# Kernel optimization log

Measured on AMD Instinct MI355X. Metric: run time of the kernel, lower is better.

The kernel has to match this reference:

```python
import jax, jax.numpy as jnp
import numpy as np
from jax import lax

H = 512   # hidden_size
R = 4     # read heads
W = 32    # memory word size
N = 64    # memory cells
B = 64    # batch
T = 256   # seq len
IFACE = R * W + 3 * W + 5 * R + 3      # 247
HID_C = H + IFACE                       # 759 controller LSTM hidden
IN_C = H + R * W                        # 640 controller LSTM input
EPS = 1e-6


def setup_inputs() -> dict:
    key = jax.random.key(0)
    ks = jax.random.split(key, 7)
    s = 0.05
    return {
        "x": jax.random.normal(ks[0], (B, T, H), jnp.float32),
        "Wih_e": jax.random.normal(ks[1], (4 * H, H), jnp.float32) * s,
        "Whh_e": jax.random.normal(ks[2], (4 * H, H), jnp.float32) * s,
        "b_e": jnp.zeros((4 * H,), jnp.float32),
        "Wih_c": jax.random.normal(ks[3], (4 * HID_C, IN_C), jnp.float32) * s,
        "Whh_c": jax.random.normal(ks[4], (4 * HID_C, HID_C), jnp.float32) * s,
        "b_c": jnp.zeros((4 * HID_C,), jnp.float32),
    }


def lstm_cell(xt, h, c, Wih, Whh, b):
    g = xt @ Wih.T + h @ Whh.T + b
    i, f, gg, o = jnp.split(g, 4, axis=-1)  # PyTorch gate order i,f,g,o
    c = jax.nn.sigmoid(f) * c + jax.nn.sigmoid(i) * jnp.tanh(gg)
    h = jax.nn.sigmoid(o) * jnp.tanh(c)
    return h, c


def content_weights(M, keys, strengths):
    # M: [B,N,W], keys: [B,K,W], strengths: [B,K] -> softmaxed similarity [B,K,N]
    Mn = M * lax.rsqrt(jnp.sum(M * M, -1, keepdims=True) + EPS)
    kn = keys * lax.rsqrt(jnp.sum(keys * keys, -1, keepdims=True) + EPS)
    sim = jnp.einsum('bkw,bnw->bkn', kn, Mn)
    return jax.nn.softmax(sim * strengths[..., None], axis=-1)


def reference(x, Wih_e, Whh_e, b_e, Wih_c, Whh_c, b_c):
    # ---- encoder LSTM over time ----
    def enc_step(carry, xt):
        h, c = carry
        h, c = lstm_cell(xt, h, c, Wih_e, Whh_e, b_e)
        return (h, c), h

    z = jnp.zeros((B, H), x.dtype)
    _, enc = lax.scan(enc_step, (z, z), x.transpose(1, 0, 2))  # [T,B,H]

    # ---- controller LSTM + DNC memory per timestep ----
    eye = jnp.eye(N, dtype=x.dtype)

    def dnc_step(carry, e_t):
        h, c, M, u, p, L, wr, ww, rv = carry
        x_t = jnp.concatenate([e_t, rv], axis=-1)          # [B, H + R*W]
        h, c = lstm_cell(x_t, h, c, Wih_c, Whh_c, b_c)
        out = h[:, :H]
        xi = h[:, H:]                                       # [B, IFACE]
        o = 0
        read_keys = jnp.tanh(xi[:, :R * W].reshape(B, R, W)); o = R * W
        read_str = jax.nn.softplus(xi[:, o:o + R]); o += R
        write_key = jnp.tanh(xi[:, o:o + W]).reshape(B, 1, W); o += W
        write_str = jax.nn.softplus(xi[:, o:o + 1]); o += 1
        erase = jax.nn.sigmoid(xi[:, o:o + W]); o += W
        write_vec = jnp.tanh(xi[:, o:o + W]); o += W
        free_g = jax.nn.sigmoid(xi[:, o:o + R]); o += R
        alloc_g = jax.nn.sigmoid(xi[:, o:o + 1]); o += 1
        write_g = jax.nn.sigmoid(xi[:, o:o + 1]); o += 1
        read_modes = jax.nn.softmax(xi[:, o:o + 3 * R].reshape(B, R, 3), -1)
        # usage + retention
        psi = jnp.prod(1.0 - free_g[..., None] * wr, axis=1)   # [B,N]
        u = (u + ww - u * ww) * psi
        # allocation weighting via sorted usage
        idx = jnp.argsort(u, axis=-1)
        su = jnp.take_along_axis(u, idx, -1)
        cp = jnp.concatenate([jnp.ones((B, 1), u.dtype), jnp.cumprod(su, -1)[:, :-1]], -1)
        a = jnp.take_along_axis((1.0 - su) * cp, jnp.argsort(idx, -1), -1)
        # write weighting
        cw = content_weights(M, write_key, write_str)[:, 0]    # [B,N]
        ww = write_g * (alloc_g * a + (1.0 - alloc_g) * cw)
        # memory write
        M = M * (1.0 - ww[..., None] * erase[:, None, :]) + ww[..., None] * write_vec[:, None, :]
        # temporal link + precedence
        L = (1.0 - ww[:, :, None] - ww[:, None, :]) * L + ww[:, :, None] * p[:, None, :]
        L = L * (1.0 - eye)
        p = (1.0 - jnp.sum(ww, -1, keepdims=True)) * p + ww
        # read weighting: backward, content, forward modes
        cr = content_weights(M, read_keys, read_str)           # [B,R,N]
        fw = jnp.einsum('bnm,brm->brn', L, wr)
        bw = jnp.einsum('bmn,brm->brn', L, wr)
        wr = read_modes[..., 0:1] * bw + read_modes[..., 1:2] * cr + read_modes[..., 2:3] * fw
        rv = jnp.einsum('brn,bnw->brw', wr, M).reshape(B, R * W)
        return (h, c, M, u, p, L, wr, ww, rv), out

    init = (
        jnp.zeros((B, HID_C), x.dtype), jnp.zeros((B, HID_C), x.dtype),
        jnp.zeros((B, N, W), x.dtype), jnp.zeros((B, N), x.dtype),
        jnp.zeros((B, N), x.dtype), jnp.zeros((B, N, N), x.dtype),
        jnp.zeros((B, R, N), x.dtype), jnp.zeros((B, N), x.dtype),
        jnp.zeros((B, R * W), x.dtype),
    )
    _, outs = lax.scan(dnc_step, init, enc)   # [T,B,H]
    return outs.transpose(1, 0, 2)            # dnc_encoded [B,T,H]
```

## Files before the change

kernel.cpp:

```cpp
#include <hip/hip_runtime.h>
#include <math.h>


#define EPSF 1e-6f

__device__ __forceinline__ float sigmoidf_(float x) { return 1.f / (1.f + expf(-x)); }
__device__ __forceinline__ float softplusf_(float x) {
    return (x > 0.f) ? x + log1pf(expf(-x)) : log1pf(expf(x));
}
__device__ __forceinline__ void stg_coh(float* p, float v) {
    __hip_atomic_store(p, v, __ATOMIC_RELAXED, __HIP_MEMORY_SCOPE_AGENT);
}
__device__ __forceinline__ void st_flag(int* p, int v) {
    __hip_atomic_store(p, v, __ATOMIC_RELAXED, __HIP_MEMORY_SCOPE_AGENT);
}
__device__ __forceinline__ int ld_flag(const int* p) {
    return __hip_atomic_load(p, __ATOMIC_RELAXED, __HIP_MEMORY_SCOPE_AGENT);
}
__device__ __forceinline__ void poll256(const int* f, int lane, int tgt) {
    const int* p = f + lane * 32;
    for (;;) {
        int a = ld_flag(p);
        int b = ld_flag(p + 64 * 32);
        int c = ld_flag(p + 128 * 32);
        int d = ld_flag(p + 192 * 32);
        if (__all(min(min(a, b), min(c, d)) >= tgt)) break;
        __builtin_amdgcn_s_sleep(2);
    }
}
__device__ __forceinline__ void pollg(const int* f, int lane, int tgt) {
    const int* p = f + (64 + lane) * 32;
    for (;;) {
        int a = ld_flag(p);
        int b = ld_flag(p + 64 * 32);
        int c = ld_flag(p + 128 * 32);
        if (__all(min(min(a, b), c) >= tgt)) break;
        __builtin_amdgcn_s_sleep(2);
    }
}
__device__ __forceinline__ void pollx(const int* f, int lane, int tgt) {
    const int* p = f + (192 + (lane < 62 ? lane : 61)) * 32;
    while (!__all(ld_flag(p) >= tgt)) __builtin_amdgcn_s_sleep(2);
}
__device__ __forceinline__ void pollm(const int* f2, int lane, int tgt) {
    while (!__all(ld_flag(f2 + lane * 32) >= tgt)) __builtin_amdgcn_s_sleep(2);
}

__global__ __launch_bounds__(256) void prep_weights(const float* __restrict__ Whh_c,
                                                    const float* __restrict__ Wih_c,
                                                    float* __restrict__ Wcat) {
    int idx = blockIdx.x * 256 + threadIdx.x;
    if (idx < 3036 * 896) {
        int r = idx / 896, j = idx - r * 896;
        float v;
        if (j < 759) v = Whh_c[r * 759 + j];
        else if (j < 768) v = 0.f;
        else v = Wih_c[r * 640 + 512 + (j - 768)];
        Wcat[idx] = v;
    }
}

__global__ __launch_bounds__(256, 2) void proj_gemm(const float* __restrict__ A,
                                                    const float* __restrict__ W,
                                                    const float* __restrict__ bias,
                                                    float* __restrict__ OUT, int Ncols,
                                                    int wstride, int arow_base, int arow_stride_t,
                                                    int arow_stride_b, int arowlen, int Mrows) {
    __shared__ float As[16 * 68];
    __shared__ float Ws[16 * 68];
    const int tid = threadIdx.x;
    const int ntile = blockIdx.x, mtile = blockIdx.y;
    const int tx = tid & 15, ty = tid >> 4;
    const int lr = tid >> 2;
    const int lk = (tid & 3) * 4;
    const size_t arow =
        (size_t)arow_base + (size_t)mtile * arow_stride_t + (size_t)lr * arow_stride_b;
    const float* aptr = A + arow * arowlen + lk;
    const int wn = ntile * 64 + lr;
    const bool wok = (wn < Ncols);
    const float* wptr = W + (size_t)(wok ? wn : 0) * wstride + lk;
    float acc[4][4] = {};
    for (int kt = 0; kt < 512; kt += 16) {
        float4 av = *(const float4*)(aptr + kt);
        float4 w4l = *(const float4*)(wptr + kt);
        if (!wok) w4l = make_float4(0.f, 0.f, 0.f, 0.f);
        __syncthreads();
        As[(lk + 0) * 68 + lr] = av.x;
        As[(lk + 1) * 68 + lr] = av.y;
        As[(lk + 2) * 68 + lr] = av.z;
        As[(lk + 3) * 68 + lr] = av.w;
        Ws[(lk + 0) * 68 + lr] = w4l.x;
        Ws[(lk + 1) * 68 + lr] = w4l.y;
        Ws[(lk + 2) * 68 + lr] = w4l.z;
        Ws[(lk + 3) * 68 + lr] = w4l.w;
        __syncthreads();
#pragma unroll
        for (int k = 0; k < 16; ++k) {
            float4 a4 = *(const float4*)&As[k * 68 + ty * 4];
            float4 w4 = *(const float4*)&Ws[k * 68 + tx * 4];
            acc[0][0] = fmaf(a4.x, w4.x, acc[0][0]);
            acc[0][1] = fmaf(a4.x, w4.y, acc[0][1]);
            acc[0][2] = fmaf(a4.x, w4.z, acc[0][2]);
            acc[0][3] = fmaf(a4.x, w4.w, acc[0][3]);
            acc[1][0] = fmaf(a4.y, w4.x, acc[1][0]);
            acc[1][1] = fmaf(a4.y, w4.y, acc[1][1]);
            acc[1][2] = fmaf(a4.y, w4.z, acc[1][2]);
            acc[1][3] = fmaf(a4.y, w4.w, acc[1][3]);
            acc[2][0] = fmaf(a4.z, w4.x, acc[2][0]);
            acc[2][1] = fmaf(a4.z, w4.y, acc[2][1]);
            acc[2][2] = fmaf(a4.z, w4.z, acc[2][2]);
            acc[2][3] = fmaf(a4.z, w4.w, acc[2][3]);
            acc[3][0] = fmaf(a4.w, w4.x, acc[3][0]);
            acc[3][1] = fmaf(a4.w, w4.y, acc[3][1]);
            acc[3][2] = fmaf(a4.w, w4.z, acc[3][2]);
            acc[3][3] = fmaf(a4.w, w4.w, acc[3][3]);
        }
    }
    const int col0 = ntile * 64 + tx * 4;
    const int row0 = mtile * 64 + ty * 4;
#pragma unroll
    for (int j = 0; j < 4; ++j) {
        int col = col0 + j;
        if (col < Ncols) {
            float bv = bias[col];
            float4 st = make_float4(acc[0][j] + bv, acc[1][j] + bv, acc[2][j] + bv,
                                    acc[3][j] + bv);
            *(float4*)&OUT[(size_t)col * Mrows + row0] = st;
        }
    }
}

__global__ __launch_bounds__(256) void enc_emit(const float* __restrict__ HSE,
                                                float* __restrict__ ENC, int t0) {
    const int tl = blockIdx.x, bgrp = blockIdx.y;
    const int c4 = threadIdx.x & 127, b = bgrp * 2 + (threadIdx.x >> 7);
    float4 v = *(const float4*)&HSE[(size_t)tl * 32768 + c4 * 256 + b * 4];
    *(float4*)&ENC[((size_t)(t0 + tl) * 64 + b) * 512 + c4 * 4] = v;
}
__global__ __launch_bounds__(256) void out_emit(const float* __restrict__ HS,
                                                float* __restrict__ OUT, int t0) {
    const int tl = blockIdx.x, bgrp = blockIdx.y;
    const int c4 = threadIdx.x & 127, b = bgrp * 2 + (threadIdx.x >> 7);
    float4 v = *(const float4*)&HS[(size_t)tl * 57344 + c4 * 256 + b * 4];
    *(float4*)&OUT[(size_t)b * 131072 + (size_t)(t0 + tl) * 512 + c4 * 4] = v;
}

__global__ __launch_bounds__(512, 1) void enc_seq(const float* __restrict__ Whh,
                                                  const float* __restrict__ XPT,
                                                  float* __restrict__ HSE,
                                                  float* __restrict__ CE, int M, int TC,
                                                  int* flags) {
    __shared__ float part[8 * 4 * 64];
    __shared__ float hstage[128 * 256];
    const int tid = threadIdx.x;
    const int bk = blockIdx.x;
    const int lane = tid & 63;
    const int wv = __builtin_amdgcn_readfirstlane(tid >> 6);
    const int q = wv & 3, cidx = wv >> 2;
    const int cell = bk + 256 * cidx;
    const float* __restrict__ w0 = Whh + ((size_t)(0 * 512 + cell)) * 512 + q * 128;
    const float* __restrict__ w1 = Whh + ((size_t)(1 * 512 + cell)) * 512 + q * 128;
    const float* __restrict__ w2 = Whh + ((size_t)(2 * 512 + cell)) * 512 + q * 128;
    const float* __restrict__ w3 = Whh + ((size_t)(3 * 512 + cell)) * 512 + q * 128;
    float c_reg = 0.f;
    if (q == 0) c_reg = CE[cell * 64 + lane];
    for (int tl = 0; tl < TC; ++tl) {
        const float* rslot = HSE + (size_t)((tl + TC - 1) % TC) * 32768;
        float* wslot = HSE + (size_t)tl * 32768;
        float x0 = 0.f, x1 = 0.f, x2 = 0.f, x3 = 0.f;
        if (q == 0) {
            const int m = tl * 64 + lane;
            x0 = XPT[(size_t)(0 * 512 + cell) * M + m];
            x1 = XPT[(size_t)(1 * 512 + cell) * M + m];
            x2 = XPT[(size_t)(2 * 512 + cell) * M + m];
            x3 = XPT[(size_t)(3 * 512 + cell) * M + m];
        }
        {
            float4* __restrict__ hs4 = (float4*)hstage;
            const float4* __restrict__ src4 = (const float4*)rslot;
#pragma unroll
            for (int k = 0; k < 16; ++k) hs4[tid + k * 512] = src4[tid + k * 512];
        }
        __syncthreads();
        float a0 = 0.f, a1 = 0.f, a2 = 0.f, a3 = 0.f;
        {
            const float4* __restrict__ hx = (const float4*)hstage + q * 32 * 64;
#pragma unroll 8
            for (int i = 0; i < 32; ++i) {
                float4 hv = hx[i * 64 + lane];
                float4 q0 = *(const float4*)&w0[i * 4];
                float4 q1 = *(const float4*)&w1[i * 4];
                float4 q2 = *(const float4*)&w2[i * 4];
                float4 q3 = *(const float4*)&w3[i * 4];
                a0 = fmaf(hv.x, q0.x, a0); a0 = fmaf(hv.y, q0.y, a0);
                a0 = fmaf(hv.z, q0.z, a0); a0 = fmaf(hv.w, q0.w, a0);
                a1 = fmaf(hv.x, q1.x, a1); a1 = fmaf(hv.y, q1.y, a1);
                a1 = fmaf(hv.z, q1.z, a1); a1 = fmaf(hv.w, q1.w, a1);
                a2 = fmaf(hv.x, q2.x, a2); a2 = fmaf(hv.y, q2.y, a2);
                a2 = fmaf(hv.z, q2.z, a2); a2 = fmaf(hv.w, q2.w, a2);
                a3 = fmaf(hv.x, q3.x, a3); a3 = fmaf(hv.y, q3.y, a3);
                a3 = fmaf(hv.z, q3.z, a3); a3 = fmaf(hv.w, q3.w, a3);
            }
        }
        part[(wv * 4 + 0) * 64 + lane] = a0;
        part[(wv * 4 + 1) * 64 + lane] = a1;
        part[(wv * 4 + 2) * 64 + lane] = a2;
        part[(wv * 4 + 3) * 64 + lane] = a3;
        __syncthreads();
        if (q == 0) {
            float g4[4];
#pragma unroll
            for (int g = 0; g < 4; ++g) {
                g4[g] = part[((cidx * 4 + 0) * 4 + g) * 64 + lane] +
                        part[((cidx * 4 + 1) * 4 + g) * 64 + lane] +
                        part[((cidx * 4 + 2) * 4 + g) * 64 + lane] +
                        part[((cidx * 4 + 3) * 4 + g) * 64 + lane];
            }
            float cc = sigmoidf_(g4[1] + x1) * c_reg + sigmoidf_(g4[0] + x0) * tanhf(g4[2] + x2);
            float hh = sigmoidf_(g4[3] + x3) * tanhf(cc);
            c_reg = cc;
            stg_coh(&wslot[(cell >> 2) * 256 + lane * 4 + (cell & 3)], hh);
        }
        __syncthreads();
        if (tid == 0) st_flag(flags + bk * 32, tl + 1);
        if (tl + 1 < TC) {
            if (wv == 0) poll256(flags, lane, tl + 1);
            __syncthreads();
        }
    }
    if (q == 0) CE[cell * 64 + lane] = c_reg;
}

__global__ __launch_bounds__(1024, 1) void dnc_seq(
    const float* __restrict__ Wcat, const float* __restrict__ CPT, float* __restrict__ HS,
    float* __restrict__ CC, float* __restrict__ Mg, float* __restrict__ Ug,
    float* __restrict__ Pg, float* __restrict__ WWg, float* __restrict__ Lg,
    float* __restrict__ WRg, int M, int TC, int* flags) {
    __shared__ float part[16 * 4 * 64];
    __shared__ float hstage[96 * 256];
    __shared__ float M_l[64 * 33];
    __shared__ float L_l[64 * 65];
    __shared__ float act[256];
    __shared__ float wr_l[256];
    __shared__ float u_l[64], p_l[64], ww_l[64], sM2[64], srt_l[64], asrt_l[64];
    __shared__ float modes_l[12], kss_l[4], scal[4];

    const int tid = threadIdx.x;
    const int bk = blockIdx.x;
    const int lane = tid & 63;
    const int wv = __builtin_amdgcn_readfirstlane(tid >> 6);
    const int q = wv & 3, cidx = wv >> 2;
    const bool machb = (bk < 64);
    const int cell_raw = machb ? 0 : (bk - 64) * 4 + cidx;
    const bool valid = !machb && (cell_raw < 759);
    const int cell = valid ? cell_raw : 0;
    const int b = bk;
    int* flags2 = flags + 8192;

    const float* __restrict__ wh0 = Wcat + (size_t)(0 * 759 + cell) * 896 + q * 96;
    const float* __restrict__ wh1 = Wcat + (size_t)(1 * 759 + cell) * 896 + q * 96;
    const float* __restrict__ wh2 = Wcat + (size_t)(2 * 759 + cell) * 896 + q * 96;
    const float* __restrict__ wh3 = Wcat + (size_t)(3 * 759 + cell) * 896 + q * 96;
    const float* __restrict__ wr0 = Wcat + (size_t)(0 * 759 + cell) * 896 + 768 + q * 32;
    const float* __restrict__ wr1 = Wcat + (size_t)(1 * 759 + cell) * 896 + 768 + q * 32;
    const float* __restrict__ wr2 = Wcat + (size_t)(2 * 759 + cell) * 896 + 768 + q * 32;
    const float* __restrict__ wr3 = Wcat + (size_t)(3 * 759 + cell) * 896 + 768 + q * 32;

    float c_reg = 0.f;
    if (valid && q == 0) c_reg = CC[cell * 64 + lane];

    if (machb) {
        if (tid < 256) {
#pragma unroll
            for (int i = 0; i < 8; ++i) {
                int e = tid + 256 * i;
                M_l[(e >> 5) * 33 + (e & 31)] = Mg[b * 2048 + e];
            }
#pragma unroll
            for (int i = 0; i < 16; ++i) {
                int e = tid + 256 * i;
                L_l[(e >> 6) * 65 + (e & 63)] = Lg[b * 4096 + e];
            }
            wr_l[tid] = WRg[b * 256 + tid];
        }
        if (tid < 64) {
            u_l[tid] = Ug[b * 64 + tid];
            p_l[tid] = Pg[b * 64 + tid];
            ww_l[tid] = WWg[b * 64 + tid];
        }
        __syncthreads();
    }

#define ACC768S(SLOT)                                                                \
    {                                                                                \
        const float4* __restrict__ src4 = (const float4*)(SLOT);                     \
        float4* __restrict__ hs4 = (float4*)hstage;                                  \
        _Pragma("unroll 1") for (int hf = 0; hf < 2; ++hf) {                         \
            _Pragma("unroll") for (int k = 0; k < 6; ++k) {                          \
                const int idx = tid + k * 1024;                                      \
                hs4[idx] = src4[hf * 6144 + idx];                                    \
            }                                                                        \
            __syncthreads();                                                         \
            if (valid) {                                                             \
                const float* __restrict__ wA0 = wh0 + hf * 384;                      \
                const float* __restrict__ wA1 = wh1 + hf * 384;                      \
                const float* __restrict__ wA2 = wh2 + hf * 384;                      \
                const float* __restrict__ wA3 = wh3 + hf * 384;                      \
                const float4* __restrict__ hx = hs4 + q * 24 * 64;                   \
                _Pragma("unroll 8") for (int i = 0; i < 24; ++i) {                   \
                    float4 hv = hx[i * 64 + lane];                                   \
                    float4 u0 = *(const float4*)&wA0[i * 4];                         \
                    float4 u1 = *(const float4*)&wA1[i * 4];                         \
                    float4 u2 = *(const float4*)&wA2[i * 4];                         \
                    float4 u3 = *(const float4*)&wA3[i * 4];                         \
                    A0 = fmaf(hv.x, u0.x, A0); A0 = fmaf(hv.y, u0.y, A0);            \
                    A0 = fmaf(hv.z, u0.z, A0); A0 = fmaf(hv.w, u0.w, A0);            \
                    A1 = fmaf(hv.x, u1.x, A1); A1 = fmaf(hv.y, u1.y, A1);            \
                    A1 = fmaf(hv.z, u1.z, A1); A1 = fmaf(hv.w, u1.w, A1);            \
                    A2 = fmaf(hv.x, u2.x, A2); A2 = fmaf(hv.y, u2.y, A2);            \
                    A2 = fmaf(hv.z, u2.z, A2); A2 = fmaf(hv.w, u2.w, A2);            \
                    A3 = fmaf(hv.x, u3.x, A3); A3 = fmaf(hv.y, u3.y, A3);            \
                    A3 = fmaf(hv.w, u3.w, A3); A3 = fmaf(hv.z, u3.z, A3);            \
                }                                                                    \
            }                                                                        \
            __syncthreads();                                                         \
        }                                                                            \
    }

    float cp0 = 0.f, cp1 = 0.f, cp2 = 0.f, cp3 = 0.f;
    if (valid && q == 0) {
        cp0 = CPT[(size_t)(0 * 759 + cell) * M + lane];
        cp1 = CPT[(size_t)(1 * 759 + cell) * M + lane];
        cp2 = CPT[(size_t)(2 * 759 + cell) * M + lane];
        cp3 = CPT[(size_t)(3 * 759 + cell) * M + lane];
    }
    float A0 = 0.f, A1 = 0.f, A2 = 0.f, A3 = 0.f;
    if (!machb) ACC768S(HS + (size_t)(TC - 1) * 57344);

    for (int tl = 0; tl < TC; ++tl) {
        const bool last = (tl + 1 == TC);
        const float* rslot = HS + (size_t)((tl + TC - 1) % TC) * 57344;
        float* wslot = HS + (size_t)tl * 57344;
        if (!machb) {
            float b0 = 0.f, b1 = 0.f, b2 = 0.f, b3 = 0.f;
            if (valid) {
                const float4* __restrict__ hx = (const float4*)rslot + (192 + q * 8) * 64;
#pragma unroll
                for (int i = 0; i < 8; ++i) {
                    float4 hv = hx[i * 64 + lane];
                    float4 u0 = *(const float4*)&wr0[i * 4];
                    float4 u1 = *(const float4*)&wr1[i * 4];
                    float4 u2 = *(const float4*)&wr2[i * 4];
                    float4 u3 = *(const float4*)&wr3[i * 4];
                    b0 = fmaf(hv.x, u0.x, b0); b0 = fmaf(hv.y, u0.y, b0);
                    b0 = fmaf(hv.z, u0.z, b0); b0 = fmaf(hv.w, u0.w, b0);
                    b1 = fmaf(hv.x, u1.x, b1); b1 = fmaf(hv.y, u1.y, b1);
                    b1 = fmaf(hv.z, u1.z, b1); b1 = fmaf(hv.w, u1.w, b1);
                    b2 = fmaf(hv.x, u2.x, b2); b2 = fmaf(hv.y, u2.y, b2);
                    b2 = fmaf(hv.z, u2.z, b2); b2 = fmaf(hv.w, u2.w, b2);
                    b3 = fmaf(hv.x, u3.x, b3); b3 = fmaf(hv.y, u3.y, b3);
                    b3 = fmaf(hv.z, u3.z, b3); b3 = fmaf(hv.w, u3.w, b3);
                }
            }
            part[(wv * 4 + 0) * 64 + lane] = A0 + b0;
            part[(wv * 4 + 1) * 64 + lane] = A1 + b1;
            part[(wv * 4 + 2) * 64 + lane] = A2 + b2;
            part[(wv * 4 + 3) * 64 + lane] = A3 + b3;
            __syncthreads();
            if (valid && q == 0) {
                float g4[4];
#pragma unroll
                for (int g = 0; g < 4; ++g) {
                    g4[g] = part[((cidx * 4 + 0) * 4 + g) * 64 + lane] +
                            part[((cidx * 4 + 1) * 4 + g) * 64 + lane] +
                            part[((cidx * 4 + 2) * 4 + g) * 64 + lane] +
                            part[((cidx * 4 + 3) * 4 + g) * 64 + lane];
                }
                float cc =
                    sigmoidf_(g4[1] + cp1) * c_reg + sigmoidf_(g4[0] + cp0) * tanhf(g4[2] + cp2);
                float hh = sigmoidf_(g4[3] + cp3) * tanhf(cc);
                c_reg = cc;
                stg_coh(&wslot[(bk - 64) * 256 + lane * 4 + cidx], hh);
            }
            __syncthreads();
            if (tid == 0) st_flag(flags + bk * 32, tl + 1);
            if (!last) {
                if (wv == 0) pollg(flags, lane, tl + 1);
                __syncthreads();
                float np0 = 0.f, np1 = 0.f, np2 = 0.f, np3 = 0.f;
                if (valid && q == 0) {
                    const int m = (tl + 1) * 64 + lane;
                    np0 = CPT[(size_t)(0 * 759 + cell) * M + m];
                    np1 = CPT[(size_t)(1 * 759 + cell) * M + m];
                    np2 = CPT[(size_t)(2 * 759 + cell) * M + m];
                    np3 = CPT[(size_t)(3 * 759 + cell) * M + m];
                }
                A0 = A1 = A2 = A3 = 0.f;
                ACC768S(wslot);
                cp0 = np0; cp1 = np1; cp2 = np2; cp3 = np3;
                if (wv == 0) pollm(flags2, lane, tl + 1);
                __syncthreads();
            }
        } else {
            if (wv == 0) pollx(flags, lane, tl + 1);
            __syncthreads();
            if (tid < 247) {
                float v = wslot[(128 + (tid >> 2)) * 256 + b * 4 + (tid & 3)];
                float a;
                if (tid < 128) a = tanhf(v);
                else if (tid < 132) a = softplusf_(v);
                else if (tid < 164) a = tanhf(v);
                else if (tid == 164) a = softplusf_(v);
                else if (tid < 197) a = sigmoidf_(v);
                else if (tid < 229) a = tanhf(v);
                else if (tid < 235) a = sigmoidf_(v);
                else a = v;
                act[tid] = a;
            }
            if (tid < 64) {
                float s2 = 0.f;
                for (int w = 0; w < 32; ++w) {
                    float mm = M_l[tid * 33 + w];
                    s2 = fmaf(mm, mm, s2);
                }
                sM2[tid] = s2;
            }
            __syncthreads();
            if (tid < 64) {
                if (tid < 4) {
                    float m0 = act[235 + 3 * tid], m1 = act[236 + 3 * tid],
                          m2 = act[237 + 3 * tid];
                    float mx = fmaxf(m0, fmaxf(m1, m2));
                    float e0 = expf(m0 - mx), e1 = expf(m1 - mx), e2 = expf(m2 - mx);
                    float s = e0 + e1 + e2;
                    modes_l[3 * tid] = e0 / s;
                    modes_l[3 * tid + 1] = e1 / s;
                    modes_l[3 * tid + 2] = e2 / s;
                    float ks = 0.f;
                    for (int w = 0; w < 32; ++w) {
                        float kk = act[tid * 32 + w];
                        ks = fmaf(kk, kk, ks);
                    }
                    kss_l[tid] = ks;
                }
                if (tid == 4) {
                    float s = 0.f;
                    for (int w = 0; w < 32; ++w) {
                        float kk = act[132 + w];
                        s = fmaf(kk, kk, s);
                    }
                    scal[0] = s;
                }
                float psi = 1.f;
#pragma unroll
                for (int r = 0; r < 4; ++r) psi *= 1.f - act[229 + r] * wr_l[r * 64 + tid];
                float un = u_l[tid], wwo = ww_l[tid];
                float unew = (un + wwo - un * wwo) * psi;
                u_l[tid] = unew;
                int rk = 0;
                for (int m = 0; m < 64; ++m) {
                    float um = u_l[m];
                    rk += (um < unew) || (um == unew && m < tid);
                }
                srt_l[rk] = unew;
                float v = srt_l[tid];
                float incl = v;
#pragma unroll
                for (int off = 1; off < 64; off <<= 1) {
                    float o = __shfl_up(incl, off);
                    if (tid >= off) incl *= o;
                }
                float excl = __shfl_up(incl, 1);
                if (tid == 0) excl = 1.f;
                asrt_l[tid] = (1.f - v) * excl;
                float dot = 0.f;
                for (int w = 0; w < 32; ++w) dot = fmaf(act[132 + w], M_l[tid * 33 + w], dot);
                float logit = dot * rsqrtf(sM2[tid] + EPSF) * rsqrtf(scal[0] + EPSF) * act[164];
                float mx = logit;
#pragma unroll
                for (int off = 32; off; off >>= 1) mx = fmaxf(mx, __shfl_xor(mx, off));
                float e = expf(logit - mx);
                float s = e;
#pragma unroll
                for (int off = 32; off; off >>= 1) s += __shfl_xor(s, off);
                float cw = e / s;
                float a = asrt_l[rk];
                float agv = act[233], wgv = act[234];
                float wn = wgv * (agv * a + (1.f - agv) * cw);
                ww_l[tid] = wn;
                float sw = wn;
#pragma unroll
                for (int off = 32; off; off >>= 1) sw += __shfl_xor(sw, off);
                if (tid == 0) scal[1] = sw;
            }
            __syncthreads();
            if (tid < 256) {
#pragma unroll
                for (int i = 0; i < 8; ++i) {
                    int e = tid + 256 * i;
                    int n = e >> 5, w = e & 31;
                    float wwn = ww_l[n];
                    M_l[n * 33 + w] =
                        M_l[n * 33 + w] * (1.f - wwn * act[165 + w]) + wwn * act[197 + w];
                }
#pragma unroll
                for (int i = 0; i < 16; ++i) {
                    int e = tid + 256 * i;
                    int n = e >> 6, m = e & 63;
                    float Lv = L_l[n * 65 + m];
                    Lv = (1.f - ww_l[n] - ww_l[m]) * Lv + ww_l[n] * p_l[m];
                    L_l[n * 65 + m] = (n == m) ? 0.f : Lv;
                }
            }
            __syncthreads();
            float wrn = 0.f;
            if (tid < 256) {
                const int r = wv;
                const int n = lane;
                if (r == 0) p_l[n] = (1.f - scal[1]) * p_l[n] + ww_l[n];
                float s2 = 0.f;
                for (int w = 0; w < 32; ++w) {
                    float mm = M_l[n * 33 + w];
                    s2 = fmaf(mm, mm, s2);
                }
                float dot = 0.f;
                for (int w = 0; w < 32; ++w) dot = fmaf(act[r * 32 + w], M_l[n * 33 + w], dot);
                float logit = dot * rsqrtf(s2 + EPSF) * rsqrtf(kss_l[r] + EPSF) * act[128 + r];
                float mx = logit;
#pragma unroll
                for (int off = 32; off; off >>= 1) mx = fmaxf(mx, __shfl_xor(mx, off));
                float e = expf(logit - mx);
                float s = e;
#pragma unroll
                for (int off = 32; off; off >>= 1) s += __shfl_xor(s, off);
                float cr = e / s;
                float fw = 0.f, bw = 0.f;
                for (int m = 0; m < 64; ++m) {
                    float wrm = wr_l[r * 64 + m];
                    fw = fmaf(L_l[n * 65 + m], wrm, fw);
                    bw = fmaf(L_l[m * 65 + n], wrm, bw);
                }
                wrn = modes_l[r * 3] * bw + modes_l[r * 3 + 1] * cr + modes_l[r * 3 + 2] * fw;
            }
            __syncthreads();
            if (tid < 256) wr_l[tid] = wrn;
            __syncthreads();
            if (tid < 128) {
                const int r = tid >> 5, w = tid & 31;
                float rv = 0.f;
                for (int n = 0; n < 64; ++n) rv = fmaf(wr_l[r * 64 + n], M_l[n * 33 + w], rv);
                stg_coh(&wslot[(192 + (tid >> 2)) * 256 + b * 4 + (tid & 3)], rv);
            }
            __syncthreads();
            if (tid == 0) st_flag(flags2 + bk * 32, tl + 1);
        }
    }
    if (valid && q == 0) CC[cell * 64 + lane] = c_reg;
    if (machb) {
        if (tid < 256) {
#pragma unroll
            for (int i = 0; i < 8; ++i) {
                int e = tid + 256 * i;
                Mg[b * 2048 + e] = M_l[(e >> 5) * 33 + (e & 31)];
            }
#pragma unroll
            for (int i = 0; i < 16; ++i) {
                int e = tid + 256 * i;
                Lg[b * 4096 + e] = L_l[(e >> 6) * 65 + (e & 63)];
            }
            WRg[b * 256 + tid] = wr_l[tid];
        }
        if (tid < 64) {
            Ug[b * 64 + tid] = u_l[tid];
            Pg[b * 64 + tid] = p_l[tid];
            WWg[b * 64 + tid] = ww_l[tid];
        }
    }
}

extern "C" void kernel_launch(void* const* d_in, const int* in_sizes, int n_in, void* d_out,
                              int out_size, void* d_ws, size_t ws_size, hipStream_t stream) {
    const float* x = (const float*)d_in[0];
    const float* Wih_e = (const float*)d_in[1];
    const float* Whh_e = (const float*)d_in[2];
    const float* b_e = (const float*)d_in[3];
    const float* Wih_c = (const float*)d_in[4];
    const float* Whh_c = (const float*)d_in[5];
    const float* b_c = (const float*)d_in[6];
    float* out = (float*)d_out;
    float* ws = (float*)d_ws;

    int TC = 64;
    while (TC > 2) {
        size_t need =
            ((size_t)11612096 + (size_t)TC * 415488 + (size_t)(512 / TC) * 16384) * 4;
        if (need <= ws_size) break;
        TC >>= 1;
    }
    const int nch = 256 / TC;
    const int M = TC * 64;

    size_t off = 0;
    float* XPT = ws + off; off += (size_t)2048 * M;
    float* CPT = ws + off; off += (size_t)3036 * M;
    float* Wcat = ws + off; off += (size_t)3036 * 896;
    float* ENC = ws + off; off += (size_t)256 * 64 * 512;
    size_t zoff = off;
    float* HSE = ws + off; off += (size_t)TC * 32768;
    float* CE = ws + off; off += 512 * 64;
    float* HS = ws + off; off += (size_t)TC * 57344;
    float* CC = ws + off; off += 759 * 64;
    float* Mg = ws + off; off += 64 * 2048;
    float* Ug = ws + off; off += 64 * 64;
    float* Pg = ws + off; off += 64 * 64;
    float* WWg = ws + off; off += 64 * 64;
    float* Lg = ws + off; off += 64 * 4096;
    float* WRg = ws + off; off += 64 * 256;
    int* BAR = (int*)(ws + off); off += (size_t)2 * nch * 16384;
    size_t zbytes = (off - zoff) * 4;

    hipMemsetAsync(ws + zoff, 0, zbytes, stream);
    prep_weights<<<dim3((3036 * 896 + 255) / 256), dim3(256), 0, stream>>>(Whh_c, Wih_c, Wcat);
    for (int c = 0; c < nch; ++c) {
        proj_gemm<<<dim3(32, TC), dim3(256), 0, stream>>>(x, Wih_e, b_e, XPT, 2048, 512, c * TC,
                                                          1, 256, 512, M);
        enc_seq<<<dim3(256), dim3(512), 0, stream>>>(Whh_e, XPT, HSE, CE, M, TC,
                                                     BAR + (size_t)c * 16384);
        enc_emit<<<dim3(TC, 32), dim3(256), 0, stream>>>(HSE, ENC, c * TC);
    }
    for (int c = 0; c < nch; ++c) {
        proj_gemm<<<dim3(48, TC), dim3(256), 0, stream>>>(ENC, Wih_c, b_c, CPT, 3036, 640,
                                                          c * TC * 64, 64, 1, 512, M);
        dnc_seq<<<dim3(256), dim3(1024), 0, stream>>>(Wcat, CPT, HS, CC, Mg, Ug, Pg, WWg, Lg,
                                                      WRg, M, TC, BAR + (size_t)(nch + c) * 16384);
        out_emit<<<dim3(TC, 32), dim3(256), 0, stream>>>(HS, out, c * TC);
    }
}
```

Measured before the change: 7.603 ms.

## Double-buffer hidden-state staging into four chunks with register prefetch

The 768-wide hidden-state reduction used to stage two halves through shared memory, each with a load-sync-compute-sync pattern. It now splits the work into four chunks with two shared buffers. The next chunk is loaded into registers while the current chunk is computed, and only one barrier is needed per chunk. The aim is to hide global-memory latency and cut barrier count on the per-timestep critical path, at the cost of more registers and a changed weight-slice mapping per wave.

Measured after the change: 7.753 ms. About the same (+2.0%).

```diff
diff --git a/kernel.cpp b/kernel.cpp
--- a/kernel.cpp
+++ b/kernel.cpp
@@ -257,10 +257,10 @@
     const int b = bk;
     int* flags2 = flags + 8192;
 
-    const float* __restrict__ wh0 = Wcat + (size_t)(0 * 759 + cell) * 896 + q * 96;
-    const float* __restrict__ wh1 = Wcat + (size_t)(1 * 759 + cell) * 896 + q * 96;
-    const float* __restrict__ wh2 = Wcat + (size_t)(2 * 759 + cell) * 896 + q * 96;
-    const float* __restrict__ wh3 = Wcat + (size_t)(3 * 759 + cell) * 896 + q * 96;
+    const float* __restrict__ wh0 = Wcat + (size_t)(0 * 759 + cell) * 896 + q * 48;
+    const float* __restrict__ wh1 = Wcat + (size_t)(1 * 759 + cell) * 896 + q * 48;
+    const float* __restrict__ wh2 = Wcat + (size_t)(2 * 759 + cell) * 896 + q * 48;
+    const float* __restrict__ wh3 = Wcat + (size_t)(3 * 759 + cell) * 896 + q * 48;
     const float* __restrict__ wr0 = Wcat + (size_t)(0 * 759 + cell) * 896 + 768 + q * 32;
     const float* __restrict__ wr1 = Wcat + (size_t)(1 * 759 + cell) * 896 + 768 + q * 32;
     const float* __restrict__ wr2 = Wcat + (size_t)(2 * 759 + cell) * 896 + 768 + q * 32;
@@ -291,23 +291,34 @@
         __syncthreads();
     }
 
-#define ACC768S(SLOT)                                                                \
+#define ACC768Q(SLOT)                                                                \
     {                                                                                \
         const float4* __restrict__ src4 = (const float4*)(SLOT);                     \
-        float4* __restrict__ hs4 = (float4*)hstage;                                  \
-        _Pragma("unroll 1") for (int hf = 0; hf < 2; ++hf) {                         \
-            _Pragma("unroll") for (int k = 0; k < 6; ++k) {                          \
-                const int idx = tid + k * 1024;                                      \
-                hs4[idx] = src4[hf * 6144 + idx];                                    \
+        float4* __restrict__ bufA = (float4*)hstage;                                 \
+        float4* __restrict__ bufB = ((float4*)hstage) + 3072;                        \
+        {                                                                            \
+            float4 r0 = src4[tid];                                                   \
+            float4 r1 = src4[tid + 1024];                                            \
+            float4 r2 = src4[tid + 2048];                                            \
+            bufA[tid] = r0; bufA[tid + 1024] = r1; bufA[tid + 2048] = r2;            \
+        }                                                                            \
+        __syncthreads();                                                             \
+        _Pragma("unroll 1") for (int s = 0; s < 4; ++s) {                            \
+            const float4* __restrict__ cur = (s & 1) ? bufB : bufA;                  \
+            float4* __restrict__ nxt = (s & 1) ? bufA : bufB;                        \
+            float4 r0, r1, r2;                                                       \
+            if (s < 3) {                                                             \
+                r0 = src4[(s + 1) * 3072 + tid];                                     \
+                r1 = src4[(s + 1) * 3072 + tid + 1024];                              \
+                r2 = src4[(s + 1) * 3072 + tid + 2048];                              \
             }                                                                        \
-            __syncthreads();                                                         \
             if (valid) {                                                             \
-                const float* __restrict__ wA0 = wh0 + hf * 384;                      \
-                const float* __restrict__ wA1 = wh1 + hf * 384;                      \
-                const float* __restrict__ wA2 = wh2 + hf * 384;                      \
-                const float* __restrict__ wA3 = wh3 + hf * 384;                      \
-                const float4* __restrict__ hx = hs4 + q * 24 * 64;                   \
-                _Pragma("unroll 8") for (int i = 0; i < 24; ++i) {                   \
+                const float* __restrict__ wA0 = wh0 + s * 192;                       \
+                const float* __restrict__ wA1 = wh1 + s * 192;                       \
+                const float* __restrict__ wA2 = wh2 + s * 192;                       \
+                const float* __restrict__ wA3 = wh3 + s * 192;                       \
+                const float4* __restrict__ hx = cur + q * 12 * 64;                   \
+                _Pragma("unroll") for (int i = 0; i < 12; ++i) {                     \
                     float4 hv = hx[i * 64 + lane];                                   \
                     float4 u0 = *(const float4*)&wA0[i * 4];                         \
                     float4 u1 = *(const float4*)&wA1[i * 4];                         \
@@ -320,10 +331,13 @@
                     A2 = fmaf(hv.x, u2.x, A2); A2 = fmaf(hv.y, u2.y, A2);            \
                     A2 = fmaf(hv.z, u2.z, A2); A2 = fmaf(hv.w, u2.w, A2);            \
                     A3 = fmaf(hv.x, u3.x, A3); A3 = fmaf(hv.y, u3.y, A3);            \
-                    A3 = fmaf(hv.w, u3.w, A3); A3 = fmaf(hv.z, u3.z, A3);            \
+                    A3 = fmaf(hv.z, u3.z, A3); A3 = fmaf(hv.w, u3.w, A3);            \
                 }                                                                    \
             }                                                                        \
-            __syncthreads();                                                         \
+            if (s < 3) {                                                             \
+                nxt[tid] = r0; nxt[tid + 1024] = r1; nxt[tid + 2048] = r2;           \
+                __syncthreads();                                                     \
+            }                                                                        \
         }                                                                            \
     }
 
@@ -335,7 +349,7 @@
         cp3 = CPT[(size_t)(3 * 759 + cell) * M + lane];
     }
     float A0 = 0.f, A1 = 0.f, A2 = 0.f, A3 = 0.f;
-    if (!machb) ACC768S(HS + (size_t)(TC - 1) * 57344);
+    if (!machb) ACC768Q(HS + (size_t)(TC - 1) * 57344);
 
     for (int tl = 0; tl < TC; ++tl) {
         const bool last = (tl + 1 == TC);
@@ -396,7 +410,7 @@
                     np3 = CPT[(size_t)(3 * 759 + cell) * M + m];
                 }
                 A0 = A1 = A2 = A3 = 0.f;
-                ACC768S(wslot);
+                ACC768Q(wslot);
                 cp0 = np0; cp1 = np1; cp2 = np2; cp3 = np3;
                 if (wv == 0) pollm(flags2, lane, tl + 1);
                 __syncthreads();
```
